# Kernel tuning notes

Measured on AMD Instinct MI355X. Metric: run time of the kernel, lower is better.

## Reference

```python
import jax, jax.numpy as jnp
from jax import lax
import numpy as np

NPOINT = 1024
RADIUS = 0.25
NSAMPLE = 32
USE_XYZ = True


def setup_inputs() -> dict:
    key = jax.random.key(0)
    k1, k2 = jax.random.split(key)
    xyz = jax.random.normal(k1, (8, 8192, 3), dtype=jnp.float32)
    points = jax.random.normal(k2, (8, 8192, 32), dtype=jnp.float32)
    return {"xyz": xyz, "points": points}


def furthest_point_sample(xyz, npoint):
    """Iterative FPS; returns (B, npoint, 3) sampled coordinates.
    Matches torch reference: seeded with xyz[:, 0], squared-distance metric."""
    B, N, _ = xyz.shape
    first = xyz[:, 0]  # (B, 3)
    d0 = jnp.full((B, N), 1e38, dtype=xyz.dtype)

    def step(carry, _):
        dist, last = carry  # dist: (B,N), last: (B,3)
        d2 = jnp.sum((xyz - last[:, None, :]) ** 2, axis=-1)  # (B,N)
        dist = jnp.minimum(dist, d2)
        idx = jnp.argmax(dist, axis=1)  # (B,)
        nxt = jnp.take_along_axis(xyz, idx[:, None, None], axis=1)[:, 0]  # (B,3)
        return (dist, nxt), nxt

    _, outs = lax.scan(step, (d0, first), None, length=npoint - 1)  # (npoint-1, B, 3)
    return jnp.concatenate([first[None], outs], axis=0).transpose(1, 0, 2)  # (B,npoint,3)


def ball_query(radius, nsample, xyz, new_xyz):
    """First `nsample` indices within `radius` of each center (ascending index
    order), padded with the first found index — matches pointnet2 CUDA kernel.
    Returns (B, npoint, nsample) int32."""
    N = xyz.shape[1]
    d2 = jnp.sum((new_xyz[:, :, None, :] - xyz[:, None, :, :]) ** 2, axis=-1)  # (B,npoint,N)
    mask = d2 < radius * radius
    ar = jnp.arange(N, dtype=jnp.int32)
    # top_k on negated indices -> smallest valid indices first
    score = jnp.where(mask, -ar, jnp.int32(-(N + 1)))
    vals, _ = lax.top_k(score, nsample)  # (B,npoint,nsample), descending
    valid = vals > -(N + 1)
    idx = jnp.where(valid, -vals, -vals[..., :1])  # pad with first hit
    return idx.astype(jnp.int32)


def group_points(points, idx):
    """points (B,N,C), idx (B,npoint,nsample) -> (B,npoint,nsample,C)."""
    B, npoint, nsample = idx.shape
    C = points.shape[-1]
    flat = idx.reshape(B, npoint * nsample)  # (B, npoint*nsample)
    g = jnp.take_along_axis(points, flat[:, :, None], axis=1)
    return g.reshape(B, npoint, nsample, C)


def reference(xyz, points):
    new_xyz = furthest_point_sample(xyz, NPOINT)  # (B,npoint,3)
    idx = ball_query(RADIUS, NSAMPLE, xyz, new_xyz)  # (B,npoint,nsample)
    grouped_xyz = group_points(xyz, idx) - new_xyz[:, :, None, :]  # center-relative
    grouped_points = group_points(points, idx)
    if USE_XYZ:
        new_points = jnp.concatenate([grouped_xyz, grouped_points], axis=-1)
    else:
        new_points = grouped_points
    return new_xyz, new_points
```

## Files before the change

### kernel.cpp

```cpp
#include <hip/hip_runtime.h>

#define BATCH   8
#define NPTS    8192
#define NPOINT  1024
#define NSAMPLE 32
#define CHANC   32
#define OUTC    35
#define R2      0.0625f

typedef float v2f __attribute__((ext_vector_type(2)));

template <int CTRL>
__device__ __forceinline__ float dpp_max_step(float v) {
    int r = __builtin_amdgcn_update_dpp(__float_as_int(v), __float_as_int(v),
                                        CTRL, 0xf, 0xf, false);
    return fmaxf(v, __int_as_float(r));
}
#define DPP_ROW_SHR(n)  (0x110 | (n))
#define DPP_BCAST15     0x142
#define DPP_BCAST31     0x143

__device__ __forceinline__ unsigned long long u64max(unsigned long long a,
                                                     unsigned long long b) {
    return a > b ? a : b;
}

__global__ __launch_bounds__(512) void fps_kernel(const float* __restrict__ xyz,
                                                  float* __restrict__ new_xyz,
                                                  float4* __restrict__ xyz4) {
#pragma clang fp contract(off)
    const int b    = blockIdx.x;
    const int t    = threadIdx.x;
    const int lane = t & 63;
    const int w    = t >> 6;
    const float* bx = xyz + (size_t)b * NPTS * 3;

    __shared__ float4 pts[NPTS];
    __shared__ unsigned long long partial[2][8];

    v2f px[8], py[8], pz[8], dist[8];
    {
        float f[48];
        float4* fq = (float4*)f;
        const float4* s4 = (const float4*)bx + t * 12;
#pragma unroll
        for (int q = 0; q < 12; ++q) fq[q] = s4[q];
#pragma unroll
        for (int p = 0; p < 8; ++p) {
            px[p] = (v2f){f[6 * p + 0], f[6 * p + 3]};
            py[p] = (v2f){f[6 * p + 1], f[6 * p + 4]};
            pz[p] = (v2f){f[6 * p + 2], f[6 * p + 5]};
            dist[p] = (v2f){1e38f, 1e38f};
        }
#pragma unroll
        for (int i = 0; i < 16; ++i) {
            const int j  = t * 16 + i;
            const int js = j ^ ((j >> 4) & 7);
            pts[js] = make_float4(f[3 * i + 0], f[3 * i + 1], f[3 * i + 2], 0.0f);
        }
    }
    __syncthreads();

    float4 c0 = pts[0];
    float lx = c0.x, ly = c0.y, lz = c0.z;
    if (t == 0) {
        float* o = new_xyz + (size_t)b * NPOINT * 3;
        o[0] = lx; o[1] = ly; o[2] = lz;
    }

    for (int s = 1; s < NPOINT; ++s) {
        const v2f lx2 = (v2f){lx, lx};
        const v2f ly2 = (v2f){ly, ly};
        const v2f lz2 = (v2f){lz, lz};
        float bestv = -1.0f;
        int   bi    = 0;
#pragma unroll
        for (int p = 0; p < 8; ++p) {
            const v2f dx = px[p] - lx2;
            const v2f dy = py[p] - ly2;
            const v2f dz = pz[p] - lz2;
            const v2f d2 = (dx * dx + dy * dy) + dz * dz;
            const float d0 = fminf(dist[p].x, d2.x);
            const float d1 = fminf(dist[p].y, d2.y);
            dist[p] = (v2f){d0, d1};
            if (d0 > bestv) { bestv = d0; bi = 2 * p; }
            if (d1 > bestv) { bestv = d1; bi = 2 * p + 1; }
        }
        const int besti = (t << 4) + bi;

        float v = bestv;
        v = dpp_max_step<DPP_ROW_SHR(1)>(v);
        v = dpp_max_step<DPP_ROW_SHR(2)>(v);
        v = dpp_max_step<DPP_ROW_SHR(4)>(v);
        v = dpp_max_step<DPP_ROW_SHR(8)>(v);
        v = dpp_max_step<DPP_BCAST15>(v);
        v = dpp_max_step<DPP_BCAST31>(v);
        const float smax = __int_as_float(__builtin_amdgcn_readlane(__float_as_int(v), 63));

        const unsigned long long m = __ballot(bestv == smax);
        const int par = s & 1;
        if (lane == (int)__builtin_ctzll(m)) {
            partial[par][w] = ((unsigned long long)__float_as_uint(smax) << 32)
                              | (unsigned)(~besti);
        }
        __syncthreads();

        const unsigned long long* P = partial[par];
        const unsigned long long a0 = P[0], a1 = P[1], a2 = P[2], a3 = P[3];
        const unsigned long long a4 = P[4], a5 = P[5], a6 = P[6], a7 = P[7];
        const unsigned long long bp =
            u64max(u64max(u64max(a0, a1), u64max(a2, a3)),
                   u64max(u64max(a4, a5), u64max(a6, a7)));
        const int idx = (int)(~(unsigned)bp);
        const int js  = idx ^ ((idx >> 4) & 7);
        const float4 cw = pts[js];
        lx = cw.x; ly = cw.y; lz = cw.z;
        if (t == 0) {
            float* o = new_xyz + ((size_t)b * NPOINT + s) * 3;
            o[0] = lx; o[1] = ly; o[2] = lz;
        }
    }

    float4* wb = xyz4 + (size_t)b * NPTS;
#pragma unroll
    for (int q = 0; q < 16; ++q) {
        const int p  = q * 512 + t;
        const int ps = p ^ ((p >> 4) & 7);
        wb[p] = pts[ps];
    }
}

__global__ __launch_bounds__(256) void ballgroup_kernel(const float4* __restrict__ xyz4,
                                                        const float* __restrict__ points,
                                                        const float* __restrict__ new_xyz,
                                                        float* __restrict__ out) {
#pragma clang fp contract(off)
    const int tid  = threadIdx.x;
    const int lane = tid & 63;
    const int r    = tid >> 6;
    const int gw   = blockIdx.x;
    const int b    = gw >> 10;

    const float4* bx4 = xyz4 + (size_t)b * NPTS;
    const float*  cen = new_xyz + (size_t)gw * 3;
    const float cx = cen[0], cy = cen[1], cz = cen[2];

    __shared__ int qidx[4][NSAMPLE];
    __shared__ int qcnt[4];

    int k = 0;
    const int qbase = r << 11;
    for (int base = qbase; base < qbase + 2048; base += 256) {
        float4 p4[4];
#pragma unroll
        for (int u = 0; u < 4; ++u) p4[u] = bx4[base + u * 64 + lane];
        bool in[4];
#pragma unroll
        for (int u = 0; u < 4; ++u) {
            const float dx = p4[u].x - cx;
            const float dy = p4[u].y - cy;
            const float dz = p4[u].z - cz;
            const float d2 = (dx * dx + dy * dy) + dz * dz;
            in[u] = d2 < R2;
        }
#pragma unroll
        for (int u = 0; u < 4; ++u) {
            const unsigned long long mu = __ballot(in[u]);
            const int pre = __popcll(mu & ((1ull << lane) - 1ull));
            if (in[u] && (k + pre) < NSAMPLE) qidx[r][k + pre] = base + u * 64 + lane;
            k += __popcll(mu);
        }
        if (k >= NSAMPLE) break;
    }
    if (k > NSAMPLE) k = NSAMPLE;
    if (lane == 0) qcnt[r] = k;
    __syncthreads();

    const int c0n = qcnt[0], c1n = qcnt[1], c2n = qcnt[2], c3n = qcnt[3];
    const int o1 = c0n, o2 = c0n + c1n, o3 = o2 + c2n;
    const int total = o3 + c3n;
    const int kk = total < NSAMPLE ? total : NSAMPLE;
    const int r0 = (c0n > 0) ? 0 : (c1n > 0) ? 1 : (c2n > 0) ? 2 : 3;
    const int firstIdx = qidx[r0][0];

    float*       o    = out + (size_t)gw * NSAMPLE * OUTC;
    const float* prow = points + (size_t)b * NPTS * CHANC;
    for (int e = tid; e < NSAMPLE * OUTC; e += 256) {
        const int s = e / OUTC;
        const int c = e - s * OUTC;
        int j;
        if (s < kk) {
            const int rr  = (int)(s >= o1) + (int)(s >= o2) + (int)(s >= o3);
            const int off = (rr == 0) ? 0 : (rr == 1) ? o1 : (rr == 2) ? o2 : o3;
            j = qidx[rr][s - off];
        } else {
            j = firstIdx;
        }
        float v;
        if (c < 3) {
            const float4 pj = bx4[j];
            const float pv = (c == 0) ? pj.x : (c == 1) ? pj.y : pj.z;
            const float cc = (c == 0) ? cx : (c == 1) ? cy : cz;
            v = pv - cc;
        } else {
            v = prow[j * CHANC + (c - 3)];
        }
        o[e] = v;
    }
}

extern "C" void kernel_launch(void* const* d_in, const int* in_sizes, int n_in,
                              void* d_out, int out_size, void* d_ws, size_t ws_size,
                              hipStream_t stream) {
    const float* xyz    = (const float*)d_in[0];
    const float* points = (const float*)d_in[1];
    float* new_xyz    = (float*)d_out;
    float* new_points = new_xyz + (size_t)BATCH * NPOINT * 3;
    float4* xyz4      = (float4*)d_ws;

    fps_kernel<<<BATCH, 512, 0, stream>>>(xyz, new_xyz, xyz4);
    ballgroup_kernel<<<BATCH * NPOINT, 256, 0, stream>>>(xyz4, points, new_xyz, new_points);
}
```

Baseline: 990.0 us.

## Split FPS per batch across eight cooperating blocks with global-memory atomic reduction

FPS now spreads each batch over 8 blocks of 256 threads (64 blocks total instead of 8), so each thread holds 4 points instead of 16. The per-step argmax is exchanged through step-tagged 64-bit slots in global memory, which every wave spins on before a DPP max reduction. This trades per-step arithmetic for a cross-block global-memory handshake on every iteration. It also assumes all 64 blocks are co-resident, otherwise the spin waits deadlock.

```diff
diff --git a/kernel.cpp b/kernel.cpp
--- a/kernel.cpp
+++ b/kernel.cpp
@@ -8,7 +8,13 @@
 #define OUTC    35
 #define R2      0.0625f
 
+#define NSUBB   8
+#define WPB     4
+#define NSLOT   (NSUBB * WPB)
+
 typedef float v2f __attribute__((ext_vector_type(2)));
+typedef unsigned long long u64;
+typedef unsigned int u32;
 
 template <int CTRL>
 __device__ __forceinline__ float dpp_max_step(float v) {
@@ -16,54 +22,81 @@
                                         CTRL, 0xf, 0xf, false);
     return fmaxf(v, __int_as_float(r));
 }
+template <int CTRL>
+__device__ __forceinline__ u64 dpp_umax64_step(u64 k) {
+    int lo = __builtin_amdgcn_update_dpp((int)(u32)k, (int)(u32)k,
+                                         CTRL, 0xf, 0xf, false);
+    int hi = __builtin_amdgcn_update_dpp((int)(u32)(k >> 32), (int)(u32)(k >> 32),
+                                         CTRL, 0xf, 0xf, false);
+    u64 r = ((u64)(u32)hi << 32) | (u64)(u32)lo;
+    return r > k ? r : k;
+}
 #define DPP_ROW_SHR(n)  (0x110 | (n))
 #define DPP_BCAST15     0x142
 #define DPP_BCAST31     0x143
 
-__device__ __forceinline__ unsigned long long u64max(unsigned long long a,
-                                                     unsigned long long b) {
-    return a > b ? a : b;
-}
-
-__global__ __launch_bounds__(512) void fps_kernel(const float* __restrict__ xyz,
+__global__ __launch_bounds__(256) void fps_kernel(const float* __restrict__ xyz,
                                                   float* __restrict__ new_xyz,
-                                                  float4* __restrict__ xyz4) {
+                                                  float4* __restrict__ xyz4,
+                                                  u64* __restrict__ slots) {
 #pragma clang fp contract(off)
-    const int b    = blockIdx.x;
+    const int blk  = blockIdx.x;
+    const int b    = blk & 7;
+    const int sub  = blk >> 3;
     const int t    = threadIdx.x;
     const int lane = t & 63;
-    const int w    = t >> 6;
+    const int wloc = t >> 6;
+    const int wid  = sub * WPB + wloc;
     const float* bx = xyz + (size_t)b * NPTS * 3;
+    u64* bslots = slots + (size_t)b * (2 * NSLOT);
 
     __shared__ float4 pts[NPTS];
-    __shared__ unsigned long long partial[2][8];
-
-    v2f px[8], py[8], pz[8], dist[8];
+
     {
-        float f[48];
+        float f[96];
         float4* fq = (float4*)f;
-        const float4* s4 = (const float4*)bx + t * 12;
-#pragma unroll
-        for (int q = 0; q < 12; ++q) fq[q] = s4[q];
-#pragma unroll
-        for (int p = 0; p < 8; ++p) {
+        const float4* s4 = (const float4*)bx + (size_t)t * 24;
+#pragma unroll
+        for (int q = 0; q < 24; ++q) fq[q] = s4[q];
+#pragma unroll
+        for (int i = 0; i < 32; ++i) {
+            const int j  = t * 32 + i;
+            const int js = j ^ ((j >> 4) & 7);
+            pts[js] = make_float4(f[3 * i + 0], f[3 * i + 1], f[3 * i + 2], 0.0f);
+        }
+    }
+
+    v2f px[2], py[2], pz[2], dist[2];
+    const int p0 = wid * 256 + (lane << 2);
+    {
+        float f[12];
+        float4* fq = (float4*)f;
+        const float4* s4 = (const float4*)(bx + (size_t)p0 * 3);
+#pragma unroll
+        for (int q = 0; q < 3; ++q) fq[q] = s4[q];
+#pragma unroll
+        for (int p = 0; p < 2; ++p) {
             px[p] = (v2f){f[6 * p + 0], f[6 * p + 3]};
             py[p] = (v2f){f[6 * p + 1], f[6 * p + 4]};
             pz[p] = (v2f){f[6 * p + 2], f[6 * p + 5]};
             dist[p] = (v2f){1e38f, 1e38f};
         }
-#pragma unroll
-        for (int i = 0; i < 16; ++i) {
-            const int j  = t * 16 + i;
-            const int js = j ^ ((j >> 4) & 7);
-            pts[js] = make_float4(f[3 * i + 0], f[3 * i + 1], f[3 * i + 2], 0.0f);
-        }
     }
     __syncthreads();
+
+    if (sub == 0) {
+        float4* wb = xyz4 + (size_t)b * NPTS;
+#pragma unroll
+        for (int q = 0; q < 32; ++q) {
+            const int p  = q * 256 + t;
+            const int ps = p ^ ((p >> 4) & 7);
+            wb[p] = pts[ps];
+        }
+    }
 
     float4 c0 = pts[0];
     float lx = c0.x, ly = c0.y, lz = c0.z;
-    if (t == 0) {
+    if (sub == 0 && t == 0) {
         float* o = new_xyz + (size_t)b * NPOINT * 3;
         o[0] = lx; o[1] = ly; o[2] = lz;
     }
@@ -75,7 +108,7 @@
         float bestv = -1.0f;
         int   bi    = 0;
 #pragma unroll
-        for (int p = 0; p < 8; ++p) {
+        for (int p = 0; p < 2; ++p) {
             const v2f dx = px[p] - lx2;
             const v2f dy = py[p] - ly2;
             const v2f dz = pz[p] - lz2;
@@ -86,7 +119,7 @@
             if (d0 > bestv) { bestv = d0; bi = 2 * p; }
             if (d1 > bestv) { bestv = d1; bi = 2 * p + 1; }
         }
-        const int besti = (t << 4) + bi;
+        const int besti = p0 + bi;
 
         float v = bestv;
         v = dpp_max_step<DPP_ROW_SHR(1)>(v);
@@ -97,36 +130,43 @@
         v = dpp_max_step<DPP_BCAST31>(v);
         const float smax = __int_as_float(__builtin_amdgcn_readlane(__float_as_int(v), 63));
 
-        const unsigned long long m = __ballot(bestv == smax);
+        const u64 m   = __ballot(bestv == smax);
         const int par = s & 1;
         if (lane == (int)__builtin_ctzll(m)) {
-            partial[par][w] = ((unsigned long long)__float_as_uint(smax) << 32)
-                              | (unsigned)(~besti);
-        }
-        __syncthreads();
-
-        const unsigned long long* P = partial[par];
-        const unsigned long long a0 = P[0], a1 = P[1], a2 = P[2], a3 = P[3];
-        const unsigned long long a4 = P[4], a5 = P[5], a6 = P[6], a7 = P[7];
-        const unsigned long long bp =
-            u64max(u64max(u64max(a0, a1), u64max(a2, a3)),
-                   u64max(u64max(a4, a5), u64max(a6, a7)));
-        const int idx = (int)(~(unsigned)bp);
+            const u64 rec = ((u64)(u32)s << 45)
+                          | ((u64)__float_as_uint(smax) << 13)
+                          | (u64)((~besti) & 0x1FFF);
+            __hip_atomic_store(&bslots[par * NSLOT + wid], rec,
+                               __ATOMIC_RELAXED, __HIP_MEMORY_SCOPE_AGENT);
+        }
+        asm volatile("" ::: "memory");
+
+        u64 key = 0;
+        if (lane < 32) {
+            u64* ps = &bslots[par * NSLOT + lane];
+            u64 rv;
+            do {
+                rv = __hip_atomic_load(ps, __ATOMIC_RELAXED, __HIP_MEMORY_SCOPE_AGENT);
+            } while (__ballot((int)(rv >> 45) == s) != 0x00000000FFFFFFFFull);
+            key = rv & ((1ull << 45) - 1);
+        }
+
+        key = dpp_umax64_step<DPP_ROW_SHR(1)>(key);
+        key = dpp_umax64_step<DPP_ROW_SHR(2)>(key);
+        key = dpp_umax64_step<DPP_ROW_SHR(4)>(key);
+        key = dpp_umax64_step<DPP_ROW_SHR(8)>(key);
+        key = dpp_umax64_step<DPP_BCAST15>(key);
+        key = dpp_umax64_step<DPP_BCAST31>(key);
+        const u32 klo = (u32)__builtin_amdgcn_readlane((int)(u32)key, 63);
+        const int idx = (int)((~klo) & 0x1FFF);
+
         const int js  = idx ^ ((idx >> 4) & 7);
         const float4 cw = pts[js];
         lx = cw.x; ly = cw.y; lz = cw.z;
-        if (t == 0) {
+        if (sub == 0 && t == 0) {
             float* o = new_xyz + ((size_t)b * NPOINT + s) * 3;
             o[0] = lx; o[1] = ly; o[2] = lz;
         }
-    }
-
-    float4* wb = xyz4 + (size_t)b * NPTS;
-#pragma unroll
-    for (int q = 0; q < 16; ++q) {
-        const int p  = q * 512 + t;
-        const int ps = p ^ ((p >> 4) & 7);
-        wb[p] = pts[ps];
     }
 }
 
@@ -217,7 +257,10 @@
     float* new_xyz    = (float*)d_out;
     float* new_points = new_xyz + (size_t)BATCH * NPOINT * 3;
     float4* xyz4      = (float4*)d_ws;
-
-    fps_kernel<<<BATCH, 512, 0, stream>>>(xyz, new_xyz, xyz4);
+    u64*    slots     = (u64*)((char*)d_ws + (size_t)BATCH * NPTS * sizeof(float4));
+
+    hipMemsetAsync(slots, 0, (size_t)BATCH * 2 * NSLOT * sizeof(u64), stream);
+
+    fps_kernel<<<BATCH * NSUBB, 256, 0, stream>>>(xyz, new_xyz, xyz4, slots);
     ballgroup_kernel<<<BATCH * NPOINT, 256, 0, stream>>>(xyz4, points, new_xyz, new_points);
 }
```

New measurement: 2.595 ms. 162% more time.

## Fuse FPS and ball-query grouping into one persistent kernel with streamed centers

Applied to the files above, without the earlier changes.

Merges the FPS kernel and the ball-group kernel into a single cooperative launch. Eight blocks run FPS and publish each sampled center to global slots tagged with a sequence number. The remaining blocks pull jobs from an atomic counter and spin until their center's tag appears, then do ball query and grouping. This overlaps the grouping work with the long serial FPS loop instead of running it afterwards. In exchange it adds a workspace memset, spin-wait polling, and reads of unpadded xyz from global memory.

```diff
diff --git a/kernel.cpp b/kernel.cpp
--- a/kernel.cpp
+++ b/kernel.cpp
@@ -8,7 +8,13 @@
 #define OUTC    35
 #define R2      0.0625f
 
+#define NBLK    256
+#define NTHR    512
+#define NJOBS   (BATCH * NPOINT / 2)
+
 typedef float v2f __attribute__((ext_vector_type(2)));
+typedef unsigned long long u64;
+typedef unsigned int u32;
 
 template <int CTRL>
 __device__ __forceinline__ float dpp_max_step(float v) {
@@ -20,192 +26,223 @@
 #define DPP_BCAST15     0x142
 #define DPP_BCAST31     0x143
 
-__device__ __forceinline__ unsigned long long u64max(unsigned long long a,
-                                                     unsigned long long b) {
-    return a > b ? a : b;
-}
-
-__global__ __launch_bounds__(512) void fps_kernel(const float* __restrict__ xyz,
-                                                  float* __restrict__ new_xyz,
-                                                  float4* __restrict__ xyz4) {
+__device__ __forceinline__ u64 u64max(u64 a, u64 b) { return a > b ? a : b; }
+
+__global__ __launch_bounds__(NTHR) void fused_kernel(
+        const float* __restrict__ xyz,
+        const float* __restrict__ points,
+        float* __restrict__ new_xyz,
+        float* __restrict__ out,
+        u64* __restrict__ slots,
+        u32* __restrict__ counter)
+{
 #pragma clang fp contract(off)
-    const int b    = blockIdx.x;
+    __shared__ float4 pts[NPTS];
+    __shared__ u64 partial[2][8];
+    __shared__ int qidx[2][4][NSAMPLE];
+    __shared__ int qcnt[2][4];
+    __shared__ int jobsh;
+
+    const int blk  = blockIdx.x;
     const int t    = threadIdx.x;
     const int lane = t & 63;
-    const int w    = t >> 6;
-    const float* bx = xyz + (size_t)b * NPTS * 3;
-
-    __shared__ float4 pts[NPTS];
-    __shared__ unsigned long long partial[2][8];
-
-    v2f px[8], py[8], pz[8], dist[8];
-    {
-        float f[48];
-        float4* fq = (float4*)f;
-        const float4* s4 = (const float4*)bx + t * 12;
-#pragma unroll
-        for (int q = 0; q < 12; ++q) fq[q] = s4[q];
-#pragma unroll
-        for (int p = 0; p < 8; ++p) {
-            px[p] = (v2f){f[6 * p + 0], f[6 * p + 3]};
-            py[p] = (v2f){f[6 * p + 1], f[6 * p + 4]};
-            pz[p] = (v2f){f[6 * p + 2], f[6 * p + 5]};
-            dist[p] = (v2f){1e38f, 1e38f};
-        }
-#pragma unroll
-        for (int i = 0; i < 16; ++i) {
-            const int j  = t * 16 + i;
-            const int js = j ^ ((j >> 4) & 7);
-            pts[js] = make_float4(f[3 * i + 0], f[3 * i + 1], f[3 * i + 2], 0.0f);
-        }
-    }
-    __syncthreads();
-
-    float4 c0 = pts[0];
-    float lx = c0.x, ly = c0.y, lz = c0.z;
-    if (t == 0) {
-        float* o = new_xyz + (size_t)b * NPOINT * 3;
-        o[0] = lx; o[1] = ly; o[2] = lz;
-    }
-
-    for (int s = 1; s < NPOINT; ++s) {
-        const v2f lx2 = (v2f){lx, lx};
-        const v2f ly2 = (v2f){ly, ly};
-        const v2f lz2 = (v2f){lz, lz};
-        float bestv = -1.0f;
-        int   bi    = 0;
-#pragma unroll
-        for (int p = 0; p < 8; ++p) {
-            const v2f dx = px[p] - lx2;
-            const v2f dy = py[p] - ly2;
-            const v2f dz = pz[p] - lz2;
-            const v2f d2 = (dx * dx + dy * dy) + dz * dz;
-            const float d0 = fminf(dist[p].x, d2.x);
-            const float d1 = fminf(dist[p].y, d2.y);
-            dist[p] = (v2f){d0, d1};
-            if (d0 > bestv) { bestv = d0; bi = 2 * p; }
-            if (d1 > bestv) { bestv = d1; bi = 2 * p + 1; }
-        }
-        const int besti = (t << 4) + bi;
-
-        float v = bestv;
-        v = dpp_max_step<DPP_ROW_SHR(1)>(v);
-        v = dpp_max_step<DPP_ROW_SHR(2)>(v);
-        v = dpp_max_step<DPP_ROW_SHR(4)>(v);
-        v = dpp_max_step<DPP_ROW_SHR(8)>(v);
-        v = dpp_max_step<DPP_BCAST15>(v);
-        v = dpp_max_step<DPP_BCAST31>(v);
-        const float smax = __int_as_float(__builtin_amdgcn_readlane(__float_as_int(v), 63));
-
-        const unsigned long long m = __ballot(bestv == smax);
-        const int par = s & 1;
-        if (lane == (int)__builtin_ctzll(m)) {
-            partial[par][w] = ((unsigned long long)__float_as_uint(smax) << 32)
-                              | (unsigned)(~besti);
+
+    if (blk < BATCH) {
+        const int b = blk;
+        const int w = t >> 6;
+        const float* bx = xyz + (size_t)b * NPTS * 3;
+        u64* bslot = slots + (size_t)b * NPOINT * 3;
+
+        v2f px[8], py[8], pz[8], dist[8];
+        {
+            float f[48];
+            float4* fq = (float4*)f;
+            const float4* s4 = (const float4*)bx + t * 12;
+#pragma unroll
+            for (int q = 0; q < 12; ++q) fq[q] = s4[q];
+#pragma unroll
+            for (int p = 0; p < 8; ++p) {
+                px[p] = (v2f){f[6 * p + 0], f[6 * p + 3]};
+                py[p] = (v2f){f[6 * p + 1], f[6 * p + 4]};
+                pz[p] = (v2f){f[6 * p + 2], f[6 * p + 5]};
+                dist[p] = (v2f){1e38f, 1e38f};
+            }
+#pragma unroll
+            for (int i = 0; i < 16; ++i) {
+                const int j  = t * 16 + i;
+                const int js = j ^ ((j >> 4) & 7);
+                pts[js] = make_float4(f[3 * i + 0], f[3 * i + 1], f[3 * i + 2], 0.0f);
+            }
         }
         __syncthreads();
 
-        const unsigned long long* P = partial[par];
-        const unsigned long long a0 = P[0], a1 = P[1], a2 = P[2], a3 = P[3];
-        const unsigned long long a4 = P[4], a5 = P[5], a6 = P[6], a7 = P[7];
-        const unsigned long long bp =
-            u64max(u64max(u64max(a0, a1), u64max(a2, a3)),
-                   u64max(u64max(a4, a5), u64max(a6, a7)));
-        const int idx = (int)(~(unsigned)bp);
-        const int js  = idx ^ ((idx >> 4) & 7);
-        const float4 cw = pts[js];
-        lx = cw.x; ly = cw.y; lz = cw.z;
+        float4 c0 = pts[0];
+        float lx = c0.x, ly = c0.y, lz = c0.z;
         if (t == 0) {
-            float* o = new_xyz + ((size_t)b * NPOINT + s) * 3;
+            float* o = new_xyz + (size_t)b * NPOINT * 3;
             o[0] = lx; o[1] = ly; o[2] = lz;
-        }
-    }
-
-    float4* wb = xyz4 + (size_t)b * NPTS;
-#pragma unroll
-    for (int q = 0; q < 16; ++q) {
-        const int p  = q * 512 + t;
-        const int ps = p ^ ((p >> 4) & 7);
-        wb[p] = pts[ps];
-    }
-}
-
-__global__ __launch_bounds__(256) void ballgroup_kernel(const float4* __restrict__ xyz4,
-                                                        const float* __restrict__ points,
-                                                        const float* __restrict__ new_xyz,
-                                                        float* __restrict__ out) {
-#pragma clang fp contract(off)
-    const int tid  = threadIdx.x;
-    const int lane = tid & 63;
-    const int r    = tid >> 6;
-    const int gw   = blockIdx.x;
-    const int b    = gw >> 10;
-
-    const float4* bx4 = xyz4 + (size_t)b * NPTS;
-    const float*  cen = new_xyz + (size_t)gw * 3;
-    const float cx = cen[0], cy = cen[1], cz = cen[2];
-
-    __shared__ int qidx[4][NSAMPLE];
-    __shared__ int qcnt[4];
-
-    int k = 0;
-    const int qbase = r << 11;
-    for (int base = qbase; base < qbase + 2048; base += 256) {
-        float4 p4[4];
-#pragma unroll
-        for (int u = 0; u < 4; ++u) p4[u] = bx4[base + u * 64 + lane];
-        bool in[4];
-#pragma unroll
-        for (int u = 0; u < 4; ++u) {
-            const float dx = p4[u].x - cx;
-            const float dy = p4[u].y - cy;
-            const float dz = p4[u].z - cz;
-            const float d2 = (dx * dx + dy * dy) + dz * dz;
-            in[u] = d2 < R2;
-        }
-#pragma unroll
-        for (int u = 0; u < 4; ++u) {
-            const unsigned long long mu = __ballot(in[u]);
-            const int pre = __popcll(mu & ((1ull << lane) - 1ull));
-            if (in[u] && (k + pre) < NSAMPLE) qidx[r][k + pre] = base + u * 64 + lane;
-            k += __popcll(mu);
-        }
-        if (k >= NSAMPLE) break;
-    }
-    if (k > NSAMPLE) k = NSAMPLE;
-    if (lane == 0) qcnt[r] = k;
-    __syncthreads();
-
-    const int c0n = qcnt[0], c1n = qcnt[1], c2n = qcnt[2], c3n = qcnt[3];
-    const int o1 = c0n, o2 = c0n + c1n, o3 = o2 + c2n;
-    const int total = o3 + c3n;
-    const int kk = total < NSAMPLE ? total : NSAMPLE;
-    const int r0 = (c0n > 0) ? 0 : (c1n > 0) ? 1 : (c2n > 0) ? 2 : 3;
-    const int firstIdx = qidx[r0][0];
-
-    float*       o    = out + (size_t)gw * NSAMPLE * OUTC;
-    const float* prow = points + (size_t)b * NPTS * CHANC;
-    for (int e = tid; e < NSAMPLE * OUTC; e += 256) {
-        const int s = e / OUTC;
-        const int c = e - s * OUTC;
-        int j;
-        if (s < kk) {
-            const int rr  = (int)(s >= o1) + (int)(s >= o2) + (int)(s >= o3);
-            const int off = (rr == 0) ? 0 : (rr == 1) ? o1 : (rr == 2) ? o2 : o3;
-            j = qidx[rr][s - off];
-        } else {
-            j = firstIdx;
-        }
-        float v;
-        if (c < 3) {
-            const float4 pj = bx4[j];
-            const float pv = (c == 0) ? pj.x : (c == 1) ? pj.y : pj.z;
-            const float cc = (c == 0) ? cx : (c == 1) ? cy : cz;
-            v = pv - cc;
-        } else {
-            v = prow[j * CHANC + (c - 3)];
-        }
-        o[e] = v;
+            const u64 tag = (u64)(u32)(b * NPOINT + 1);
+            __hip_atomic_store(&bslot[0], (tag << 32) | (u64)__float_as_uint(lx),
+                               __ATOMIC_RELAXED, __HIP_MEMORY_SCOPE_AGENT);
+            __hip_atomic_store(&bslot[1], (tag << 32) | (u64)__float_as_uint(ly),
+                               __ATOMIC_RELAXED, __HIP_MEMORY_SCOPE_AGENT);
+            __hip_atomic_store(&bslot[2], (tag << 32) | (u64)__float_as_uint(lz),
+                               __ATOMIC_RELAXED, __HIP_MEMORY_SCOPE_AGENT);
+        }
+
+        for (int s = 1; s < NPOINT; ++s) {
+            const v2f lx2 = (v2f){lx, lx};
+            const v2f ly2 = (v2f){ly, ly};
+            const v2f lz2 = (v2f){lz, lz};
+            float bestv = -1.0f;
+            int   bi    = 0;
+#pragma unroll
+            for (int p = 0; p < 8; ++p) {
+                const v2f dx = px[p] - lx2;
+                const v2f dy = py[p] - ly2;
+                const v2f dz = pz[p] - lz2;
+                const v2f d2 = (dx * dx + dy * dy) + dz * dz;
+                const float d0 = fminf(dist[p].x, d2.x);
+                const float d1 = fminf(dist[p].y, d2.y);
+                dist[p] = (v2f){d0, d1};
+                if (d0 > bestv) { bestv = d0; bi = 2 * p; }
+                if (d1 > bestv) { bestv = d1; bi = 2 * p + 1; }
+            }
+            const int besti = (t << 4) + bi;
+
+            float v = bestv;
+            v = dpp_max_step<DPP_ROW_SHR(1)>(v);
+            v = dpp_max_step<DPP_ROW_SHR(2)>(v);
+            v = dpp_max_step<DPP_ROW_SHR(4)>(v);
+            v = dpp_max_step<DPP_ROW_SHR(8)>(v);
+            v = dpp_max_step<DPP_BCAST15>(v);
+            v = dpp_max_step<DPP_BCAST31>(v);
+            const float smax = __int_as_float(__builtin_amdgcn_readlane(__float_as_int(v), 63));
+
+            const u64 m   = __ballot(bestv == smax);
+            const int par = s & 1;
+            if (lane == (int)__builtin_ctzll(m)) {
+                partial[par][w] = ((u64)__float_as_uint(smax) << 32)
+                                  | (unsigned)(~besti);
+            }
+            __syncthreads();
+
+            const u64* P = partial[par];
+            const u64 a0 = P[0], a1 = P[1], a2 = P[2], a3 = P[3];
+            const u64 a4 = P[4], a5 = P[5], a6 = P[6], a7 = P[7];
+            const u64 bp =
+                u64max(u64max(u64max(a0, a1), u64max(a2, a3)),
+                       u64max(u64max(a4, a5), u64max(a6, a7)));
+            const int idx = (int)(~(unsigned)bp);
+            const int js  = idx ^ ((idx >> 4) & 7);
+            const float4 cw = pts[js];
+            lx = cw.x; ly = cw.y; lz = cw.z;
+            if (t == 0) {
+                float* o = new_xyz + ((size_t)b * NPOINT + s) * 3;
+                o[0] = lx; o[1] = ly; o[2] = lz;
+                const u64 tag = (u64)(u32)(b * NPOINT + s + 1);
+                __hip_atomic_store(&bslot[3 * s + 0], (tag << 32) | (u64)__float_as_uint(lx),
+                                   __ATOMIC_RELAXED, __HIP_MEMORY_SCOPE_AGENT);
+                __hip_atomic_store(&bslot[3 * s + 1], (tag << 32) | (u64)__float_as_uint(ly),
+                                   __ATOMIC_RELAXED, __HIP_MEMORY_SCOPE_AGENT);
+                __hip_atomic_store(&bslot[3 * s + 2], (tag << 32) | (u64)__float_as_uint(lz),
+                                   __ATOMIC_RELAXED, __HIP_MEMORY_SCOPE_AGENT);
+            }
+        }
+    } else {
+        for (;;) {
+            if (t == 0) jobsh = (int)atomicAdd(counter, 1u);
+            __syncthreads();
+            const int job = jobsh;
+            if (job >= NJOBS) break;
+
+            const int half = t >> 8;
+            const int gw   = job * 2 + half;
+            const int bb   = gw >> 10;
+            const int r    = (t >> 6) & 3;
+
+            const u32 tag = (u32)(gw + 1);
+            u64* sl = slots + (size_t)gw * 3;
+            u64 w0, w1, w2;
+            for (;;) {
+                w0 = __hip_atomic_load(&sl[0], __ATOMIC_RELAXED, __HIP_MEMORY_SCOPE_AGENT);
+                w1 = __hip_atomic_load(&sl[1], __ATOMIC_RELAXED, __HIP_MEMORY_SCOPE_AGENT);
+                w2 = __hip_atomic_load(&sl[2], __ATOMIC_RELAXED, __HIP_MEMORY_SCOPE_AGENT);
+                if ((u32)(w0 >> 32) == tag && (u32)(w1 >> 32) == tag &&
+                    (u32)(w2 >> 32) == tag) break;
+                __builtin_amdgcn_s_sleep(8);
+            }
+            const float cx = __uint_as_float((u32)w0);
+            const float cy = __uint_as_float((u32)w1);
+            const float cz = __uint_as_float((u32)w2);
+
+            const float* bxr = xyz + (size_t)bb * NPTS * 3;
+            int k = 0;
+            const int qbase = r << 11;
+            for (int base = qbase; base < qbase + 2048; base += 256) {
+                float qx[4], qy[4], qz[4];
+#pragma unroll
+                for (int u = 0; u < 4; ++u) {
+                    const int j = base + u * 64 + lane;
+                    qx[u] = bxr[3 * j + 0];
+                    qy[u] = bxr[3 * j + 1];
+                    qz[u] = bxr[3 * j + 2];
+                }
+                bool in[4];
+#pragma unroll
+                for (int u = 0; u < 4; ++u) {
+                    const float dx = qx[u] - cx;
+                    const float dy = qy[u] - cy;
+                    const float dz = qz[u] - cz;
+                    const float d2 = (dx * dx + dy * dy) + dz * dz;
+                    in[u] = d2 < R2;
+                }
+#pragma unroll
+                for (int u = 0; u < 4; ++u) {
+                    const u64 mu = __ballot(in[u]);
+                    const int pre = __popcll(mu & ((1ull << lane) - 1ull));
+                    if (in[u] && (k + pre) < NSAMPLE) qidx[half][r][k + pre] = base + u * 64 + lane;
+                    k += __popcll(mu);
+                }
+                if (k >= NSAMPLE) break;
+            }
+            if (k > NSAMPLE) k = NSAMPLE;
+            if (lane == 0) qcnt[half][r] = k;
+            __syncthreads();
+
+            const int c0n = qcnt[half][0], c1n = qcnt[half][1];
+            const int c2n = qcnt[half][2], c3n = qcnt[half][3];
+            const int o1 = c0n, o2 = c0n + c1n, o3 = o2 + c2n;
+            const int total = o3 + c3n;
+            const int kk = total < NSAMPLE ? total : NSAMPLE;
+            const int rq = (c0n > 0) ? 0 : (c1n > 0) ? 1 : (c2n > 0) ? 2 : 3;
+            const int firstIdx = qidx[half][rq][0];
+
+            float*       o    = out + (size_t)gw * NSAMPLE * OUTC;
+            const float* prow = points + (size_t)bb * NPTS * CHANC;
+            const int t256 = t & 255;
+            for (int e = t256; e < NSAMPLE * OUTC; e += 256) {
+                const int sI = e / OUTC;
+                const int c  = e - sI * OUTC;
+                int j;
+                if (sI < kk) {
+                    const int rr  = (int)(sI >= o1) + (int)(sI >= o2) + (int)(sI >= o3);
+                    const int off = (rr == 0) ? 0 : (rr == 1) ? o1 : (rr == 2) ? o2 : o3;
+                    j = qidx[half][rr][sI - off];
+                } else {
+                    j = firstIdx;
+                }
+                float v;
+                if (c < 3) {
+                    const float pv = bxr[3 * j + c];
+                    const float cc = (c == 0) ? cx : (c == 1) ? cy : cz;
+                    v = pv - cc;
+                } else {
+                    v = prow[j * CHANC + (c - 3)];
+                }
+                o[e] = v;
+            }
+        }
     }
 }
 
@@ -216,8 +253,14 @@
     const float* points = (const float*)d_in[1];
     float* new_xyz    = (float*)d_out;
     float* new_points = new_xyz + (size_t)BATCH * NPOINT * 3;
-    float4* xyz4      = (float4*)d_ws;
-
-    fps_kernel<<<BATCH, 512, 0, stream>>>(xyz, new_xyz, xyz4);
-    ballgroup_kernel<<<BATCH * NPOINT, 256, 0, stream>>>(xyz4, points, new_xyz, new_points);
+
+    u64* slots   = (u64*)d_ws;
+    u32* counter = (u32*)((char*)d_ws + (size_t)BATCH * NPOINT * 3 * sizeof(u64));
+
+    hipMemsetAsync(d_ws, 0, (size_t)BATCH * NPOINT * 3 * sizeof(u64) + 64, stream);
+
+    void* args[] = { (void*)&xyz, (void*)&points, (void*)&new_xyz,
+                     (void*)&new_points, (void*)&slots, (void*)&counter };
+    hipLaunchCooperativeKernel((void*)fused_kernel, dim3(NBLK), dim3(NTHR),
+                               args, 0, stream);
 }
```

Measured after the change: 1.018 ms. +2.8%, slower.
